# Kernel optimization log

Hardware: AMD Instinct MI355X
Metric: run time of the kernel (lower is better)

## Reference

```python
import jax, jax.numpy as jnp
import numpy as np

B, S_SRC, D, H, DH, FF, L, V, W, NG = 2, 4093, 768, 12, 64, 3072, 2, 50265, 256, 3
S = S_SRC + NG            # 4096, multiple of one-sided window W=256
NC = S // W               # 16 chunks
EPS = 1e-5
CLS_IDS = (50261, 50262, 50263)
NEG = -1e9


def setup_inputs() -> dict:
    key = jax.random.key(0)
    ks = jax.random.split(key, 16)
    std = 0.02
    inp = {
        "src": jax.random.randint(ks[0], (B, S_SRC), 0, 50260),
        "mask_src": jnp.ones((B, S_SRC), dtype=bool),
        "cluster_sizes": jax.random.randint(ks[1], (B,), 0, 16),
        "word_emb": jax.random.normal(ks[2], (V, D), jnp.float32) * std,
        "pos_emb": jax.random.normal(ks[3], (S, D), jnp.float32) * std,
        "emb_ln": jnp.stack([jnp.ones((D,)), jnp.zeros((D,))]),              # [2,D] scale,bias
        "attn_w": jax.random.normal(ks[4], (L, 7, D, D), jnp.float32) * std,  # q,k,v,qg,kg,vg,o
        "attn_b": jnp.zeros((L, 7, D), jnp.float32),
        "ln_p": jnp.stack([jnp.stack([jnp.ones((D,)), jnp.zeros((D,)), jnp.ones((D,)), jnp.zeros((D,))]) for _ in range(L)]),  # [L,4,D]
        "ffn_w1": jax.random.normal(ks[5], (L, D, FF), jnp.float32) * std,
        "ffn_b1": jnp.zeros((L, FF), jnp.float32),
        "ffn_w2": jax.random.normal(ks[6], (L, FF, D), jnp.float32) * std,
        "ffn_b2": jnp.zeros((L, D), jnp.float32),
        "cls_w": jax.random.normal(ks[7], (3, D), jnp.float32) * std,
        "cls_b": jnp.zeros((3,), jnp.float32),
    }
    return inp


def _ln(x, scale, bias):
    mu = jnp.mean(x, axis=-1, keepdims=True)
    var = jnp.mean(jnp.square(x - mu), axis=-1, keepdims=True)
    return (x - mu) * jax.lax.rsqrt(var + EPS) * scale + bias


def _encoder(ids, mask, word_emb, pos_emb, emb_ln, attn_w, attn_b, ln_p,
             ffn_w1, ffn_b1, ffn_w2, ffn_b2):
    x = _ln(word_emb[ids] + pos_emb[None, :S], emb_ln[0], emb_ln[1])  # [B,S,D]

    # static banded-attention index structure (chunk of W queries sees 3W keys)
    idx = np.arange(NC)[:, None] * W + np.arange(3 * W)[None, :]  # into padded seq
    kp = idx - W                                                   # absolute key pos
    valid = (kp >= 0) & (kp < S)
    kpc = jnp.asarray(np.clip(kp, 0, S - 1))
    qpos = np.arange(W)[:, None]
    band = jnp.asarray(np.abs(np.arange(3 * W)[None, :] - W - qpos) <= W)  # [W,3W]
    # global & padding keys removed from windowed attention (HF semantics)
    keymask = mask[:, kpc] & jnp.asarray(valid)[None] & jnp.asarray(kp >= NG)[None]  # [B,NC,3W]
    allowed = band[None, None] & keymask[:, :, None, :]  # [B,NC,W,3W]
    scale = 1.0 / np.sqrt(DH)

    def layer(x, p):
        aw, ab, lnp, w1, b1, w2, b2 = p
        def proj(i):
            return (x @ aw[i] + ab[i]).reshape(B, S, H, DH).transpose(0, 2, 1, 3)
        q = proj(0) * scale
        k = proj(1)
        v = proj(2)
        kpad = jnp.pad(k, ((0, 0), (0, 0), (W, W), (0, 0)))
        vpad = jnp.pad(v, ((0, 0), (0, 0), (W, W), (0, 0)))
        Kc = kpad[:, :, kpc + W]  # [B,H,NC,3W,DH] (kpc+W indexes padded)
        Vc = vpad[:, :, kpc + W]
        qc = q.reshape(B, H, NC, W, DH)
        s_loc = jnp.einsum('bhcqd,bhckd->bhcqk', qc, Kc)
        s_loc = jnp.where(allowed[:, None], s_loc, NEG)
        s_glb = jnp.einsum('bhcqd,bhgd->bhcqg', qc, k[:, :, :NG])  # all tokens -> global keys
        probs = jax.nn.softmax(jnp.concatenate([s_glb, s_loc], axis=-1), axis=-1)
        out = (jnp.einsum('bhcqg,bhgd->bhcqd', probs[..., :NG], v[:, :, :NG])
               + jnp.einsum('bhcqk,bhckd->bhcqd', probs[..., NG:], Vc))
        out = out.reshape(B, H, S, DH)
        # global query rows: full attention with global q/k/v projections
        qg = ((x[:, :NG] @ aw[3] + ab[3]).reshape(B, NG, H, DH)) * scale
        kg = (x @ aw[4] + ab[4]).reshape(B, S, H, DH)
        vg = (x @ aw[5] + ab[5]).reshape(B, S, H, DH)
        sg = jnp.einsum('bghd,bshd->bhgs', qg, kg)
        sg = jnp.where(mask[:, None, None, :], sg, NEG)
        og = jnp.einsum('bhgs,bshd->bhgd', jax.nn.softmax(sg, axis=-1), vg)
        out = out.at[:, :, :NG, :].set(og)
        out = out.transpose(0, 2, 1, 3).reshape(B, S, D)
        xa = _ln(x + out @ aw[6] + ab[6], lnp[0], lnp[1])
        h = jax.nn.gelu(xa @ w1 + b1, approximate=False)
        return _ln(xa + h @ w2 + b2, lnp[2], lnp[3]), None

    x, _ = jax.lax.scan(layer, x, (attn_w, attn_b, ln_p, ffn_w1, ffn_b1, ffn_w2, ffn_b2))
    return x


def reference(src, mask_src, cluster_sizes, word_emb, pos_emb, emb_ln, attn_w,
              attn_b, ln_p, ffn_w1, ffn_b1, ffn_w2, ffn_b2, cls_w, cls_b):
    ids = jnp.concatenate([jnp.broadcast_to(jnp.asarray(CLS_IDS), (B, NG)), src], axis=1)
    mask = jnp.concatenate([jnp.ones((B, NG), dtype=bool), mask_src], axis=1)
    h = _encoder(ids, mask, word_emb, pos_emb, emb_ln, attn_w, attn_b, ln_p,
                 ffn_w1, ffn_b1, ffn_w2, ffn_b2)  # [B,S,D]
    mf = mask.astype(h.dtype)
    scores = [jax.nn.sigmoid(h[:, i] @ cls_w[i] + cls_b[i]) * mf[:, i] for i in range(3)]
    verd, pros, cons = (s[:, None] for s in scores)
    return verd, pros, cons, mf[:, 0][:, None]
```

## Files before the change

kernel.cpp:

```cpp
#include <hip/hip_runtime.h>
#include <hip/hip_bf16.h>
#include <math.h>

#define B_    2
#define SSRC_ 4093
#define D_    768
#define H_    12
#define DH_   64
#define FF_   3072
#define NG_   3
#define W_    256
#define S_    4096
#define NC_   16
#define NSPLIT_ 16
#define QB_   128

typedef __attribute__((ext_vector_type(8))) short frag_ab;
typedef __attribute__((ext_vector_type(4))) float f32x4;

#define GL16(gp, lp) __builtin_amdgcn_global_load_lds( \
    (const __attribute__((address_space(1))) void*)(gp), \
    (__attribute__((address_space(3))) void*)(lp), 16, 0, 0)

__device__ __forceinline__ float bflo(unsigned int w) {
    union { float f; unsigned int i; } c; c.i = w << 16; return c.f;
}
__device__ __forceinline__ float bfhi(unsigned int w) {
    union { float f; unsigned int i; } c; c.i = w & 0xffff0000u; return c.f;
}
__device__ __forceinline__ void unp8(uint4 t, float* o) {
    o[0] = bflo(t.x); o[1] = bfhi(t.x); o[2] = bflo(t.y); o[3] = bfhi(t.y);
    o[4] = bflo(t.z); o[5] = bfhi(t.z); o[6] = bflo(t.w); o[7] = bfhi(t.w);
}
__device__ __forceinline__ unsigned short f2bfu(float x) {
    __hip_bfloat16 h = __float2bfloat16(x);
    return *reinterpret_cast<unsigned short*>(&h);
}

__device__ __forceinline__ float block_sum(float v, float* red) {
    int tid = threadIdx.x;
    red[tid] = v;
    __syncthreads();
#pragma unroll
    for (int off = 128; off >= 1; off >>= 1) {
        if (tid < off) red[tid] += red[tid + off];
        __syncthreads();
    }
    float r = red[0];
    __syncthreads();
    return r;
}

__device__ __forceinline__ float block_max(float v, float* red) {
    int tid = threadIdx.x;
    red[tid] = v;
    __syncthreads();
#pragma unroll
    for (int off = 128; off >= 1; off >>= 1) {
        if (tid < off) red[tid] = fmaxf(red[tid], red[tid + off]);
        __syncthreads();
    }
    float r = red[0];
    __syncthreads();
    return r;
}

__device__ __forceinline__ void storeO(float* p, float v) { *p = v; }
__device__ __forceinline__ void storeO(__hip_bfloat16* p, float v) { *p = __float2bfloat16(v); }

__global__ __launch_bounds__(256) void embed_ln_k(
    const int* __restrict__ src, const float* __restrict__ we,
    const float* __restrict__ pe, const float* __restrict__ gam,
    const float* __restrict__ bet, float* __restrict__ X,
    __hip_bfloat16* __restrict__ Xb) {
    __shared__ float red[256];
    int row = blockIdx.x;
    int b = row >> 12;
    int s = row & (S_ - 1);
    int tid = threadIdx.x;
    int id = (s < NG_) ? (50261 + s) : src[b * SSRC_ + (s - NG_)];
    const float* wr = we + (size_t)id * D_;
    const float* pr = pe + (size_t)s * D_;
    float v[3];
    float lsum = 0.f;
#pragma unroll
    for (int j = 0; j < 3; ++j) {
        int c = tid + j * 256;
        v[j] = wr[c] + pr[c];
        lsum += v[j];
    }
    float mu = block_sum(lsum, red) * (1.0f / 768.0f);
    float ls2 = 0.f;
#pragma unroll
    for (int j = 0; j < 3; ++j) { float d = v[j] - mu; ls2 += d * d; }
    float var = block_sum(ls2, red) * (1.0f / 768.0f);
    float rs = rsqrtf(var + 1e-5f);
    float* xr = X + (size_t)row * D_;
    __hip_bfloat16* xbr = Xb + (size_t)row * D_;
#pragma unroll
    for (int j = 0; j < 3; ++j) {
        int c = tid + j * 256;
        float o = (v[j] - mu) * rs * gam[c] + bet[c];
        xr[c] = o;
        xbr[c] = __float2bfloat16(o);
    }
}

__global__ __launch_bounds__(256) void residual_ln_k(
    const float* __restrict__ x, const float* __restrict__ y,
    const float* __restrict__ y2, const float* __restrict__ gam,
    const float* __restrict__ bet, float* __restrict__ out,
    __hip_bfloat16* __restrict__ outb) {
    __shared__ float red[256];
    int row = blockIdx.x;
    int tid = threadIdx.x;
    const float* xr = x + (size_t)row * D_;
    const float* yr = y + (size_t)row * D_;
    const float* y2r = y2 ? y2 + (size_t)row * D_ : nullptr;
    float v[3];
    float lsum = 0.f;
#pragma unroll
    for (int j = 0; j < 3; ++j) {
        int c = tid + j * 256;
        v[j] = xr[c] + yr[c];
        if (y2r) v[j] += y2r[c];
        lsum += v[j];
    }
    float mu = block_sum(lsum, red) * (1.0f / 768.0f);
    float ls2 = 0.f;
#pragma unroll
    for (int j = 0; j < 3; ++j) { float d = v[j] - mu; ls2 += d * d; }
    float var = block_sum(ls2, red) * (1.0f / 768.0f);
    float rs = rsqrtf(var + 1e-5f);
    float* orow = out + (size_t)row * D_;
    __hip_bfloat16* obr = outb ? outb + (size_t)row * D_ : nullptr;
#pragma unroll
    for (int j = 0; j < 3; ++j) {
        int c = tid + j * 256;
        float o = (v[j] - mu) * rs * gam[c] + bet[c];
        orow[c] = o;
        if (obr) obr[c] = __float2bfloat16(o);
    }
}

__global__ __launch_bounds__(256) void convt_k(
    const float* __restrict__ W, __hip_bfloat16* __restrict__ WT,
    int K, int N, int npb ) {
    __shared__ float tile[32][33];
    int mat = blockIdx.x / npb;
    int bx = blockIdx.x - mat * npb;
    int by = blockIdx.y;
    const float* Wm = W + (size_t)mat * K * N;
    __hip_bfloat16* WTm = WT + (size_t)mat * N * K;
    int tx = threadIdx.x & 31, ty = threadIdx.x >> 5;
#pragma unroll
    for (int i = 0; i < 32; i += 8)
        tile[ty + i][tx] = Wm[(size_t)(by * 32 + ty + i) * N + bx * 32 + tx];
    __syncthreads();
#pragma unroll
    for (int i = 0; i < 32; i += 8)
        WTm[(size_t)(bx * 32 + ty + i) * K + by * 32 + tx] = __float2bfloat16(tile[tx][ty + i]);
}

__global__ void pack_bias_k(const float* __restrict__ ab, float* __restrict__ dst) {
    int j = blockIdx.x * 256 + threadIdx.x;
    if (j >= 5 * 768) return;
    int mat = j / 768, c = j - mat * 768;
    int i = (mat < 3) ? mat : mat + 1;
    dst[j] = ab[i * 768 + c];
}

template <int EPI, int SPLIT>
__global__ __launch_bounds__(256) void mfma_gemm_k(
    const __hip_bfloat16* __restrict__ A, const __hip_bfloat16* __restrict__ BT,
    const float* __restrict__ bias, void* __restrict__ Cout,
    int M, int N, int K, size_t matstride) {
    __shared__ __align__(16) __hip_bfloat16 As[2][4096];
    __shared__ __align__(16) __hip_bfloat16 Bs[2][4096];
    int tid = threadIdx.x;
    int lane = tid & 63;
    int w = tid >> 6, wr = w >> 1, wc = w & 1;
    int nwg = gridDim.x * gridDim.y;
    int id = blockIdx.y * gridDim.x + blockIdx.x;
    if ((nwg & 7) == 0) {
        int per = nwg >> 3;
        id = (id & 7) * per + (id >> 3);
    }
    int bx = id % gridDim.x, by = id / gridDim.x;
    int brow = by * 128, bcol = bx * 128;
    int z = blockIdx.z, nz = gridDim.z;
    int Kz = K / nz;
    int r0 = tid >> 2, k0 = (tid & 3) * 8;
    const __hip_bfloat16* Ag0 = A + (size_t)(brow + r0) * K + z * Kz + k0;
    const __hip_bfloat16* Ag1 = Ag0 + (size_t)64 * K;
    const __hip_bfloat16* Bg0 = BT + (size_t)(bcol + r0) * K + z * Kz + k0;
    const __hip_bfloat16* Bg1 = Bg0 + (size_t)64 * K;

    f32x4 acc[4][4];
#pragma unroll
    for (int m = 0; m < 4; ++m)
#pragma unroll
        for (int n = 0; n < 4; ++n) acc[m][n] = (f32x4){0.f, 0.f, 0.f, 0.f};

    int l15 = lane & 15, kb = lane >> 4;
    int aoff = (wr * 64 + l15) * 32 + kb * 8;
    int boff = (wc * 64 + l15) * 32 + kb * 8;

    int nt = Kz >> 5;
    GL16(Ag0, &As[0][tid * 8]);
    GL16(Ag1, &As[0][tid * 8 + 2048]);
    GL16(Bg0, &Bs[0][tid * 8]);
    GL16(Bg1, &Bs[0][tid * 8 + 2048]);
    __syncthreads();

    for (int t = 0; t < nt; ++t) {
        int cur = t & 1;
        if (t + 1 < nt) {
            int nxt = cur ^ 1;
            int kt = (t + 1) << 5;
            GL16(Ag0 + kt, &As[nxt][tid * 8]);
            GL16(Ag1 + kt, &As[nxt][tid * 8 + 2048]);
            GL16(Bg0 + kt, &Bs[nxt][tid * 8]);
            GL16(Bg1 + kt, &Bs[nxt][tid * 8 + 2048]);
        }
        frag_ab af[4], bf[4];
#pragma unroll
        for (int m = 0; m < 4; ++m) af[m] = *(const frag_ab*)&As[cur][aoff + m * 512];
#pragma unroll
        for (int n = 0; n < 4; ++n) bf[n] = *(const frag_ab*)&Bs[cur][boff + n * 512];
        __builtin_amdgcn_s_setprio(1);
#pragma unroll
        for (int m = 0; m < 4; ++m)
#pragma unroll
            for (int n = 0; n < 4; ++n)
                acc[m][n] = __builtin_amdgcn_mfma_f32_16x16x32_bf16(af[m], bf[n], acc[m][n], 0, 0, 0);
        __builtin_amdgcn_s_setprio(0);
        __syncthreads();
    }

    size_t zoff = (size_t)z * M * N;
#pragma unroll
    for (int m = 0; m < 4; ++m) {
        int rowb = brow + wr * 64 + m * 16 + (lane >> 4) * 4;
#pragma unroll
        for (int n = 0; n < 4; ++n) {
            int col = bcol + wc * 64 + n * 16 + l15;
            float bv = (z == 0) ? bias[col] : 0.f;
#pragma unroll
            for (int r = 0; r < 4; ++r) {
                float v = acc[m][n][r] + bv;
                size_t idx;
                if (SPLIT) {
                    int mat = col / 768;
                    idx = (size_t)mat * matstride + (size_t)(rowb + r) * 768 + (col - mat * 768);
                } else {
                    idx = zoff + (size_t)(rowb + r) * N + col;
                }
                if (EPI == 0) {
                    ((float*)Cout)[idx] = v;
                } else if (EPI == 1) {
                    ((__hip_bfloat16*)Cout)[idx] = __float2bfloat16(v);
                } else {
                    float g = 0.5f * v * (1.0f + erff(v * 0.70710678118654752f));
                    ((__hip_bfloat16*)Cout)[idx] = __float2bfloat16(g);
                }
            }
        }
    }
}

__global__ __launch_bounds__(256) void skinny_gemm_k(
    const float* __restrict__ A, const float* __restrict__ W,
    float* __restrict__ partial, int N, int K) {
    __shared__ float Asl[6][64];
    __shared__ float red[4][6][64];
    int tid = threadIdx.x;
    int cl = tid & 63;
    int kg = tid >> 6;
    int col = blockIdx.x * 64 + cl;
    int k0 = blockIdx.y * 64;
    for (int i = tid; i < 6 * 64; i += 256)
        Asl[i >> 6][i & 63] = A[(size_t)(i >> 6) * K + k0 + (i & 63)];
    __syncthreads();
    float acc[6] = {0.f, 0.f, 0.f, 0.f, 0.f, 0.f};
#pragma unroll
    for (int kk = 0; kk < 16; ++kk) {
        int k = kg * 16 + kk;
        float wv = W[(size_t)(k0 + k) * N + col];
#pragma unroll
        for (int m = 0; m < 6; ++m) acc[m] += Asl[m][k] * wv;
    }
#pragma unroll
    for (int m = 0; m < 6; ++m) red[kg][m][cl] = acc[m];
    __syncthreads();
    for (int i = tid; i < 6 * 64; i += 256) {
        int m = i >> 6, lane = i & 63;
        float s = red[0][m][lane] + red[1][m][lane] + red[2][m][lane] + red[3][m][lane];
        partial[(size_t)blockIdx.y * 6 * N + (size_t)m * N + blockIdx.x * 64 + lane] = s;
    }
}

__global__ __launch_bounds__(256) void skinny_reduce_k(
    const float* __restrict__ partial, const float* __restrict__ bias,
    float* __restrict__ outp, int N, int KS, int gelu) {
    int idx = blockIdx.x * 256 + threadIdx.x;
    if (idx >= 6 * N) return;
    int m = idx / N, col = idx - m * N;
    float s = bias[col];
    for (int kb = 0; kb < KS; ++kb)
        s += partial[(size_t)kb * 6 * N + (size_t)m * N + col];
    if (gelu) s = 0.5f * s * (1.0f + erff(s * 0.70710678118654752f));
    outp[(size_t)m * N + col] = s;
}

__global__ __launch_bounds__(256, 1) void local_attn_k(
    const __hip_bfloat16* __restrict__ Q, const __hip_bfloat16* __restrict__ K,
    const __hip_bfloat16* __restrict__ V, __hip_bfloat16* __restrict__ O) {
    __shared__ __align__(16) __hip_bfloat16 K_lds[64 * 72];
    __shared__ __align__(16) __hip_bfloat16 VT_lds[64 * 72];
    __shared__ __align__(16) __hip_bfloat16 P_lds[4][16 * 72];

    const int cq = blockIdx.x, h = blockIdx.y, b = blockIdx.z;
    const int tid = threadIdx.x;
    const int lane = tid & 63;
    const int w = tid >> 6;
    const int l15 = lane & 15, g4 = lane >> 4;
    const int cbase = cq * QB_;

    frag_ab qf[2][2];
#pragma unroll
    for (int qt = 0; qt < 2; ++qt) {
        int qa = cbase + w * 32 + qt * 16 + l15;
        const __hip_bfloat16* qp = Q + (size_t)(b * S_ + qa) * D_ + h * DH_ + g4 * 8;
        qf[qt][0] = *(const frag_ab*)qp;
        qf[qt][1] = *(const frag_ab*)(qp + 32);
    }

    f32x4 o[2][4];
#pragma unroll
    for (int qt = 0; qt < 2; ++qt)
#pragma unroll
        for (int dt = 0; dt < 4; ++dt) o[qt][dt] = (f32x4){0.f, 0.f, 0.f, 0.f};
    float mrun[2] = {-1e30f, -1e30f};
    float lrun[2] = {0.f, 0.f};

    int kw0 = cbase - W_; if (kw0 < 0) kw0 = 0;
    int kw1 = cbase + QB_ + W_; if (kw1 > S_) kw1 = S_;
    int ntiles = (kw1 - kw0) >> 6;

    char* Pw = (char*)P_lds[w];

    for (int t = 0; t < ntiles; ++t) {
        int k0 = kw0 + t * 64;
        __syncthreads();
        {
            const __hip_bfloat16* Kg = K + (size_t)(b * S_ + k0) * D_ + h * DH_;
            const __hip_bfloat16* Vg = V + (size_t)(b * S_ + k0) * D_ + h * DH_;
#pragma unroll
            for (int it = 0; it < 2; ++it) {
                int idx = tid + it * 256;
                int kk = idx >> 3, d0 = (idx & 7) * 8;
                uint4 kv = *(const uint4*)(Kg + (size_t)kk * D_ + d0);
                *(uint4*)&K_lds[kk * 72 + d0] = kv;
                uint4 vv = *(const uint4*)(Vg + (size_t)kk * D_ + d0);
                unsigned short vs[8];
                *(uint4*)vs = vv;
#pragma unroll
                for (int j = 0; j < 8; ++j) {
                    int dd = d0 + j;
                    int boff = dd * 144 + ((kk * 2) ^ (((dd >> 3) & 7) << 4));
                    *(unsigned short*)((char*)VT_lds + boff) = vs[j];
                }
            }
        }
        __syncthreads();

        frag_ab kf[4][2];
#pragma unroll
        for (int kt = 0; kt < 4; ++kt) {
            const char* kp = (const char*)K_lds + (kt * 16 + l15) * 144 + g4 * 16;
            kf[kt][0] = *(const frag_ab*)kp;
            kf[kt][1] = *(const frag_ab*)(kp + 64);
        }
        frag_ab vf[4][2];
#pragma unroll
        for (int dt = 0; dt < 4; ++dt) {
            int drow = dt * 16 + l15;
            int swz = ((drow >> 3) & 7) << 4;
            const char* vp = (const char*)VT_lds + drow * 144;
            vf[dt][0] = *(const frag_ab*)(vp + ((g4 * 16) ^ swz));
            vf[dt][1] = *(const frag_ab*)(vp + ((g4 * 16 + 64) ^ swz));
        }

#pragma unroll
        for (int qt = 0; qt < 2; ++qt) {
            f32x4 st[4];
            __builtin_amdgcn_s_setprio(1);
#pragma unroll
            for (int kt = 0; kt < 4; ++kt) {
                f32x4 z = (f32x4){0.f, 0.f, 0.f, 0.f};
                z = __builtin_amdgcn_mfma_f32_16x16x32_bf16(kf[kt][0], qf[qt][0], z, 0, 0, 0);
                z = __builtin_amdgcn_mfma_f32_16x16x32_bf16(kf[kt][1], qf[qt][1], z, 0, 0, 0);
                st[kt] = z;
            }
            __builtin_amdgcn_s_setprio(0);
            int qa = cbase + w * 32 + qt * 16 + l15;
            float sv[16];
            float mx = -1e30f;
#pragma unroll
            for (int kt = 0; kt < 4; ++kt)
#pragma unroll
                for (int r = 0; r < 4; ++r) {
                    int ka = k0 + kt * 16 + g4 * 4 + r;
                    float s = st[kt][r] * 0.125f;
                    bool bad = (ka < NG_) | (ka - qa > W_) | (qa - ka > W_);
                    s = bad ? -1e30f : s;
                    sv[kt * 4 + r] = s;
                    mx = fmaxf(mx, s);
                }
            mx = fmaxf(mx, __shfl_xor(mx, 16));
            mx = fmaxf(mx, __shfl_xor(mx, 32));
            float mnew = fmaxf(fmaxf(mrun[qt], mx), -60.0f);
            if (__any(mnew != mrun[qt])) {
                float fsc = __expf(mrun[qt] - mnew);
                mrun[qt] = mnew;
#pragma unroll
                for (int dt = 0; dt < 4; ++dt) o[qt][dt] *= fsc;
                lrun[qt] *= fsc;
            }
            float psum = 0.f;
            unsigned short pb[16];
#pragma unroll
            for (int i = 0; i < 16; ++i) {
                float p = __expf(sv[i] - mrun[qt]);
                psum += p;
                pb[i] = f2bfu(p);
            }
            psum += __shfl_xor(psum, 16);
            psum += __shfl_xor(psum, 32);
            lrun[qt] += psum;
#pragma unroll
            for (int kt = 0; kt < 4; ++kt)
#pragma unroll
                for (int rp = 0; rp < 2; ++rp) {
                    unsigned vpk = (unsigned)pb[kt * 4 + rp * 2] | ((unsigned)pb[kt * 4 + rp * 2 + 1] << 16);
                    int kloc = kt * 16 + g4 * 4 + rp * 2;
                    *(unsigned*)(Pw + l15 * 144 + kloc * 2) = vpk;
                }
            frag_ab pf0 = *(const frag_ab*)(Pw + l15 * 144 + g4 * 16);
            frag_ab pf1 = *(const frag_ab*)(Pw + l15 * 144 + g4 * 16 + 64);
            __builtin_amdgcn_s_setprio(1);
#pragma unroll
            for (int dt = 0; dt < 4; ++dt) {
                o[qt][dt] = __builtin_amdgcn_mfma_f32_16x16x32_bf16(vf[dt][0], pf0, o[qt][dt], 0, 0, 0);
                o[qt][dt] = __builtin_amdgcn_mfma_f32_16x16x32_bf16(vf[dt][1], pf1, o[qt][dt], 0, 0, 0);
            }
            __builtin_amdgcn_s_setprio(0);
        }
    }

    uint4 kgc[3][2];
    uint2 vgd[3][4];
#pragma unroll
    for (int gk = 0; gk < NG_; ++gk) {
        const __hip_bfloat16* kp = K + (size_t)(b * S_ + gk) * D_ + h * DH_ + g4 * 8;
        kgc[gk][0] = *(const uint4*)kp;
        kgc[gk][1] = *(const uint4*)(kp + 32);
        const __hip_bfloat16* vp = V + (size_t)(b * S_ + gk) * D_ + h * DH_ + g4 * 4;
#pragma unroll
        for (int dt = 0; dt < 4; ++dt)
            vgd[gk][dt] = *(const uint2*)(vp + dt * 16);
    }
#pragma unroll
    for (int qt = 0; qt < 2; ++qt) {
        float sg[3];
#pragma unroll
        for (int gk = 0; gk < NG_; ++gk) {
            float part = 0.f;
#pragma unroll
            for (int s = 0; s < 2; ++s) {
                uint4 qw = *(uint4*)&qf[qt][s];
                uint4 kw = kgc[gk][s];
                part += bflo(qw.x) * bflo(kw.x) + bfhi(qw.x) * bfhi(kw.x);
                part += bflo(qw.y) * bflo(kw.y) + bfhi(qw.y) * bfhi(kw.y);
                part += bflo(qw.z) * bflo(kw.z) + bfhi(qw.z) * bfhi(kw.z);
                part += bflo(qw.w) * bflo(kw.w) + bfhi(qw.w) * bfhi(kw.w);
            }
            part += __shfl_xor(part, 16);
            part += __shfl_xor(part, 32);
            sg[gk] = part * 0.125f;
        }
        float mx3 = fmaxf(fmaxf(sg[0], sg[1]), sg[2]);
        float mnew = fmaxf(fmaxf(mrun[qt], mx3), -60.0f);
        float fsc = __expf(mrun[qt] - mnew);
        mrun[qt] = mnew;
#pragma unroll
        for (int dt = 0; dt < 4; ++dt) o[qt][dt] *= fsc;
        lrun[qt] *= fsc;
        float pg[3];
        float psum = 0.f;
#pragma unroll
        for (int gk = 0; gk < NG_; ++gk) { pg[gk] = __expf(sg[gk] - mnew); psum += pg[gk]; }
        lrun[qt] += psum;
#pragma unroll
        for (int dt = 0; dt < 4; ++dt) {
#pragma unroll
            for (int gk = 0; gk < NG_; ++gk) {
                uint2 vv = vgd[gk][dt];
                o[qt][dt][0] += pg[gk] * bflo(vv.x);
                o[qt][dt][1] += pg[gk] * bfhi(vv.x);
                o[qt][dt][2] += pg[gk] * bflo(vv.y);
                o[qt][dt][3] += pg[gk] * bfhi(vv.y);
            }
        }
    }

#pragma unroll
    for (int qt = 0; qt < 2; ++qt) {
        float linv = 1.0f / lrun[qt];
        int qa = cbase + w * 32 + qt * 16 + l15;
        __hip_bfloat16* orow = O + (size_t)(b * S_ + qa) * D_ + h * DH_;
#pragma unroll
        for (int dt = 0; dt < 4; ++dt) {
            unsigned short pk[4];
#pragma unroll
            for (int r = 0; r < 4; ++r) pk[r] = f2bfu(o[qt][dt][r] * linv);
            *(uint2*)(orow + dt * 16 + g4 * 4) = *(uint2*)pk;
        }
    }
}

__global__ __launch_bounds__(256) void gattn_part_k(
    const float* __restrict__ qg, const __hip_bfloat16* __restrict__ KG,
    const __hip_bfloat16* __restrict__ VG, float* __restrict__ gpart) {
    __shared__ float sc[256];
    __shared__ float qs[DH_];
    __shared__ float red[256];
    __shared__ float rv[16][64];
    int split = blockIdx.x;
    int gh = blockIdx.y;
    int g = gh / H_, h = gh - g * H_;
    int b = blockIdx.z;
    int tid = threadIdx.x;
    if (tid < DH_) qs[tid] = qg[(size_t)(b * NG_ + g) * D_ + h * DH_ + tid] * 0.125f;
    __syncthreads();
    int s0 = split * (S_ / NSPLIT_);
    float acc = 0.f;
    {
        const __hip_bfloat16* kp = KG + (size_t)(b * S_ + s0 + tid) * D_ + h * DH_;
#pragma unroll
        for (int c8 = 0; c8 < 8; ++c8) {
            uint4 t = *(const uint4*)(kp + c8 * 8);
            float f[8]; unp8(t, f);
#pragma unroll
            for (int j = 0; j < 8; ++j) acc += qs[c8 * 8 + j] * f[j];
        }
    }
    float m = block_max(acc, red);
    float e = __expf(acc - m);
    sc[tid] = e;
    float l = block_sum(e, red);
    int sgq = tid >> 4, dq = (tid & 15) * 4;
    float a0 = 0.f, a1 = 0.f, a2 = 0.f, a3 = 0.f;
    const __hip_bfloat16* vbase = VG + (size_t)(b * S_ + s0 + sgq * 16) * D_ + h * DH_ + dq;
#pragma unroll
    for (int i = 0; i < 16; ++i) {
        float p = sc[sgq * 16 + i];
        uint2 vv = *(const uint2*)(vbase + (size_t)i * D_);
        a0 += p * bflo(vv.x); a1 += p * bfhi(vv.x);
        a2 += p * bflo(vv.y); a3 += p * bfhi(vv.y);
    }
    rv[sgq][dq] = a0; rv[sgq][dq + 1] = a1; rv[sgq][dq + 2] = a2; rv[sgq][dq + 3] = a3;
    __syncthreads();
    float* op = gpart + ((size_t)((b * NG_ + g) * H_ + h) * NSPLIT_ + split) * 66;
    if (tid == 0) { op[0] = m; op[1] = l; }
    if (tid < DH_) {
        float s = 0.f;
#pragma unroll
        for (int j = 0; j < 16; ++j) s += rv[j][tid];
        op[2 + tid] = s;
    }
}

template <typename TO>
__global__ __launch_bounds__(64) void gattn_comb_k(
    const float* __restrict__ gpart, TO* __restrict__ outp, int rowStride) {
    int g = blockIdx.x, h = blockIdx.y, b = blockIdx.z;
    int tid = threadIdx.x;
    const float* base = gpart + (size_t)((b * NG_ + g) * H_ + h) * NSPLIT_ * 66;
    float M = -1e30f;
#pragma unroll
    for (int p = 0; p < NSPLIT_; ++p) M = fmaxf(M, base[p * 66]);
    float l = 0.f, o = 0.f;
#pragma unroll
    for (int p = 0; p < NSPLIT_; ++p) {
        float wgt = __expf(base[p * 66] - M);
        l += wgt * base[p * 66 + 1];
        o += wgt * base[p * 66 + 2 + tid];
    }
    storeO(&outp[(size_t)(b * rowStride + g) * D_ + h * DH_ + tid], o / l);
}

__global__ void gather6_k(const float* __restrict__ X, float* __restrict__ xg) {
    int r = blockIdx.x;
    int b = r / NG_, g = r % NG_;
    for (int c = threadIdx.x; c < D_; c += blockDim.x)
        xg[(size_t)r * D_ + c] = X[(size_t)(b * S_ + g) * D_ + c];
}

__global__ __launch_bounds__(256) void classifier_k(
    const float* __restrict__ x26, const float* __restrict__ cw,
    const float* __restrict__ cb, float* __restrict__ out) {
    __shared__ float red[256];
    int tid = threadIdx.x;
    for (int i = 0; i < 3; ++i) {
        for (int b = 0; b < B_; ++b) {
            const float* xr = x26 + (size_t)(b * NG_ + i) * D_;
            const float* wr = cw + (size_t)i * D_;
            float p = 0.f;
            for (int c = tid; c < D_; c += 256) p += xr[c] * wr[c];
            float dotv = block_sum(p, red);
            if (tid == 0) out[i * B_ + b] = 1.0f / (1.0f + __expf(-(dotv + cb[i])));
        }
    }
    if (tid == 0) { out[6] = 1.0f; out[7] = 1.0f; }
}

extern "C" void kernel_launch(void* const* d_in, const int* in_sizes, int n_in,
                              void* d_out, int out_size, void* d_ws, size_t ws_size,
                              hipStream_t stream) {
    const int*   src      = (const int*)d_in[0];
    const float* word_emb = (const float*)d_in[3];
    const float* pos_emb  = (const float*)d_in[4];
    const float* emb_ln   = (const float*)d_in[5];
    const float* attn_w   = (const float*)d_in[6];
    const float* attn_b   = (const float*)d_in[7];
    const float* ln_p     = (const float*)d_in[8];
    const float* ffn_w1   = (const float*)d_in[9];
    const float* ffn_b1   = (const float*)d_in[10];
    const float* ffn_w2   = (const float*)d_in[11];
    const float* ffn_b2   = (const float*)d_in[12];
    const float* cls_w    = (const float*)d_in[13];
    const float* cls_b    = (const float*)d_in[14];
    float* out = (float*)d_out;

    const size_t NT = (size_t)B_ * S_ * D_;
    float* base = (float*)d_ws;
    float* X  = base;
    float* P4 = base + NT;
    __hip_bfloat16* Xb  = (__hip_bfloat16*)(base + 2 * NT);
    __hip_bfloat16* Qb  = (__hip_bfloat16*)(base + 5 * NT / 2);
    __hip_bfloat16* Kb  = (__hip_bfloat16*)(base + 3 * NT);
    __hip_bfloat16* Vb  = (__hip_bfloat16*)(base + 7 * NT / 2);
    __hip_bfloat16* KGb = (__hip_bfloat16*)(base + 4 * NT);
    __hip_bfloat16* VGb = (__hip_bfloat16*)(base + 9 * NT / 2);
    __hip_bfloat16* AOb = (__hip_bfloat16*)(base + 5 * NT);
    __hip_bfloat16* HCb = (__hip_bfloat16*)(base + 11 * NT / 2);
    float* pj1 = base + 15 * NT / 2;
    float* pj2 = base + 17 * NT / 2;
    __hip_bfloat16* wq5 = (__hip_bfloat16*)(base + 19 * NT / 2);
    __hip_bfloat16* wo  = wq5 + 5 * 589824;
    __hip_bfloat16* wg1 = wo + 589824;
    __hip_bfloat16* wf1 = wg1 + 2 * 589824;
    __hip_bfloat16* wf2 = wf1 + 2359296;
    float* SM  = (float*)(wf2 + 2359296);
    float* xg  = SM;
    float* qg6 = xg + 6 * D_;
    float* og6 = qg6 + 6 * D_;
    float* pr6 = og6 + 6 * D_;
    float* xa6 = pr6 + 6 * D_;
    float* h6  = xa6 + 6 * D_;
    float* f6  = h6 + 6 * FF_;
    float* x26 = f6 + 6 * D_;
    float* bias5 = x26 + 6 * D_;
    float* part = bias5 + 5 * D_;
    float* gpart = part;

    const int M = B_ * S_;
    dim3 blk(256);

    auto aw = [&](int l, int i) { return attn_w + ((size_t)(l * 7 + i)) * D_ * D_; };
    auto ab = [&](int l, int i) { return attn_b + (size_t)(l * 7 + i) * D_; };
    auto lnp = [&](int l, int i) { return ln_p + (size_t)(l * 4 + i) * D_; };

    auto skinny = [&](const float* A6, const float* Wm, const float* bias,
                      float* out6, int N, int K, int gelu) {
        skinny_gemm_k<<<dim3(N / 64, K / 64), blk, 0, stream>>>(A6, Wm, part, N, K);
        skinny_reduce_k<<<dim3((6 * N + 255) / 256), blk, 0, stream>>>(part, bias, out6, N, K / 64, gelu);
    };

    embed_ln_k<<<M, blk, 0, stream>>>(src, word_emb, pos_emb, emb_ln, emb_ln + D_, X, Xb);

    convt_k<<<dim3(24 * 3, 24), blk, 0, stream>>>(aw(0, 0), wq5, D_, D_, 24);
    convt_k<<<dim3(24 * 2, 24), blk, 0, stream>>>(aw(0, 4), wq5 + 3 * 589824, D_, D_, 24);
    pack_bias_k<<<15, blk, 0, stream>>>(ab(0, 0), bias5);
    mfma_gemm_k<1, 1><<<dim3(3840 / 128, 64), blk, 0, stream>>>(Xb, wq5, bias5, Qb, M, 3840, D_, NT);
    local_attn_k<<<dim3(S_ / QB_, H_, B_), blk, 0, stream>>>(Qb, Kb, Vb, AOb);
    gather6_k<<<B_ * NG_, blk, 0, stream>>>(X, xg);
    skinny(xg, aw(0, 3), ab(0, 3), qg6, D_, D_, 0);
    gattn_part_k<<<dim3(NSPLIT_, NG_ * H_, B_), blk, 0, stream>>>(qg6, KGb, VGb, gpart);
    gattn_comb_k<__hip_bfloat16><<<dim3(NG_, H_, B_), dim3(64), 0, stream>>>(gpart, AOb, S_);
    convt_k<<<dim3(24, 24), blk, 0, stream>>>(aw(0, 6), wo, D_, D_, 24);
    mfma_gemm_k<0, 0><<<dim3(6, 64, 2), blk, 0, stream>>>(AOb, wo, ab(0, 6), pj1, M, D_, D_, 0);
    residual_ln_k<<<M, blk, 0, stream>>>(X, pj1, pj2, lnp(0, 0), lnp(0, 1), P4, Xb);
    convt_k<<<dim3(96, 24), blk, 0, stream>>>(ffn_w1, wf1, D_, FF_, 96);
    convt_k<<<dim3(24, 96), blk, 0, stream>>>(ffn_w2, wf2, FF_, D_, 24);
    mfma_gemm_k<2, 0><<<dim3(24, 64), blk, 0, stream>>>(Xb, wf1, ffn_b1, HCb, M, FF_, D_, 0);
    mfma_gemm_k<0, 0><<<dim3(6, 64, 2), blk, 0, stream>>>(HCb, wf2, ffn_b2, pj1, M, D_, FF_, 0);
    residual_ln_k<<<M, blk, 0, stream>>>(P4, pj1, pj2, lnp(0, 2), lnp(0, 3), X, Xb);

    convt_k<<<dim3(24 * 2, 24), blk, 0, stream>>>(aw(1, 4), wg1, D_, D_, 24);
    mfma_gemm_k<1, 1><<<dim3(1536 / 128, 64), blk, 0, stream>>>(Xb, wg1, ab(1, 4), KGb, M, 1536, D_, NT);
    gather6_k<<<B_ * NG_, blk, 0, stream>>>(X, xg);
    skinny(xg, aw(1, 3), ab(1, 3), qg6, D_, D_, 0);
    gattn_part_k<<<dim3(NSPLIT_, NG_ * H_, B_), blk, 0, stream>>>(qg6, KGb, VGb, gpart);
    gattn_comb_k<float><<<dim3(NG_, H_, B_), dim3(64), 0, stream>>>(gpart, og6, NG_);
    skinny(og6, aw(1, 6), ab(1, 6), pr6, D_, D_, 0);
    residual_ln_k<<<B_ * NG_, blk, 0, stream>>>(xg, pr6, nullptr, lnp(1, 0), lnp(1, 1), xa6, nullptr);
    skinny(xa6, ffn_w1 + (size_t)D_ * FF_, ffn_b1 + FF_, h6, FF_, D_, 1);
    skinny(h6, ffn_w2 + (size_t)FF_ * D_, ffn_b2 + D_, f6, D_, FF_, 0);
    residual_ln_k<<<B_ * NG_, blk, 0, stream>>>(xa6, f6, nullptr, lnp(1, 2), lnp(1, 3), x26, nullptr);
    classifier_k<<<1, blk, 0, stream>>>(x26, cls_w, cls_b, out);
}
```

Before: 504.9 us.

## Add 256x256-tile MFMA GEMM for QKV and FFN1 projections

Introduces a 512-thread GEMM kernel with 256x256 output tiles, double-buffered LDS loads via global_load_lds, and an XCD-aware block remap. It replaces the 128-tile GEMM for the fused QKV/global projection and the FFN up-projection with GELU. Larger tiles raise arithmetic intensity and cut redundant global loads, but use more registers and LDS per block and launch fewer workgroups (15x32 and 12x32), which may reduce occupancy and leave CUs less evenly loaded.

New measurement: 537.4 us. +6.4%, slower.

```diff
diff --git a/kernel.cpp b/kernel.cpp
--- a/kernel.cpp
+++ b/kernel.cpp
@@ -255,6 +255,103 @@
                     idx = (size_t)mat * matstride + (size_t)(rowb + r) * 768 + (col - mat * 768);
                 } else {
                     idx = zoff + (size_t)(rowb + r) * N + col;
+                }
+                if (EPI == 0) {
+                    ((float*)Cout)[idx] = v;
+                } else if (EPI == 1) {
+                    ((__hip_bfloat16*)Cout)[idx] = __float2bfloat16(v);
+                } else {
+                    float g = 0.5f * v * (1.0f + erff(v * 0.70710678118654752f));
+                    ((__hip_bfloat16*)Cout)[idx] = __float2bfloat16(g);
+                }
+            }
+        }
+    }
+}
+
+template <int EPI, int SPLIT>
+__global__ __launch_bounds__(512) void mfma_gemm256_k(
+    const __hip_bfloat16* __restrict__ A, const __hip_bfloat16* __restrict__ BT,
+    const float* __restrict__ bias, void* __restrict__ Cout,
+    int M, int N, int K, size_t matstride) {
+    __shared__ __align__(16) __hip_bfloat16 As[2][8192];
+    __shared__ __align__(16) __hip_bfloat16 Bs[2][8192];
+    int tid = threadIdx.x;
+    int lane = tid & 63;
+    int w = tid >> 6;
+    int wr = w >> 2, wc = w & 3;
+    int nwg = gridDim.x * gridDim.y;
+    int id = blockIdx.y * gridDim.x + blockIdx.x;
+    if ((nwg & 7) == 0) {
+        int per = nwg >> 3;
+        id = (id & 7) * per + (id >> 3);
+    }
+    int bx = id % gridDim.x, by = id / gridDim.x;
+    int brow = by * 256, bcol = bx * 256;
+    int r0 = tid >> 2, k0 = (tid & 3) * 8;
+    const __hip_bfloat16* Ag0 = A + (size_t)(brow + r0) * K + k0;
+    const __hip_bfloat16* Ag1 = Ag0 + (size_t)128 * K;
+    const __hip_bfloat16* Bg0 = BT + (size_t)(bcol + r0) * K + k0;
+    const __hip_bfloat16* Bg1 = Bg0 + (size_t)128 * K;
+
+    f32x4 acc[8][4];
+#pragma unroll
+    for (int m = 0; m < 8; ++m)
+#pragma unroll
+        for (int n = 0; n < 4; ++n) acc[m][n] = (f32x4){0.f, 0.f, 0.f, 0.f};
+
+    int l15 = lane & 15, kb = lane >> 4;
+    int aoff = (wr * 128 + l15) * 32 + kb * 8;
+    int boff = (wc * 64 + l15) * 32 + kb * 8;
+
+    int nt = K >> 5;
+    GL16(Ag0, &As[0][tid * 8]);
+    GL16(Ag1, &As[0][tid * 8 + 4096]);
+    GL16(Bg0, &Bs[0][tid * 8]);
+    GL16(Bg1, &Bs[0][tid * 8 + 4096]);
+    __syncthreads();
+
+    for (int t = 0; t < nt; ++t) {
+        int cur = t & 1;
+        if (t + 1 < nt) {
+            int nxt = cur ^ 1;
+            int kt = (t + 1) << 5;
+            GL16(Ag0 + kt, &As[nxt][tid * 8]);
+            GL16(Ag1 + kt, &As[nxt][tid * 8 + 4096]);
+            GL16(Bg0 + kt, &Bs[nxt][tid * 8]);
+            GL16(Bg1 + kt, &Bs[nxt][tid * 8 + 4096]);
+        }
+        frag_ab bf[4];
+#pragma unroll
+        for (int n = 0; n < 4; ++n) bf[n] = *(const frag_ab*)&Bs[cur][boff + n * 512];
+        __builtin_amdgcn_s_setprio(1);
+#pragma unroll
+        for (int m = 0; m < 8; ++m) {
+            frag_ab af = *(const frag_ab*)&As[cur][aoff + m * 512];
+#pragma unroll
+            for (int n = 0; n < 4; ++n)
+                acc[m][n] = __builtin_amdgcn_mfma_f32_16x16x32_bf16(af, bf[n], acc[m][n], 0, 0, 0);
+        }
+        __builtin_amdgcn_s_setprio(0);
+        __syncthreads();
+    }
+
+#pragma unroll
+    for (int m = 0; m < 8; ++m) {
+        int rowb = brow + wr * 128 + m * 16 + (lane >> 4) * 4;
+#pragma unroll
+        for (int n = 0; n < 4; ++n) {
+            int col = bcol + wc * 64 + n * 16 + l15;
+            float bv = bias[col];
+#pragma unroll
+            for (int r = 0; r < 4; ++r) {
+                float v = acc[m][n][r] + bv;
+                size_t idx;
+                if (SPLIT) {
+                    int mat = col / 768;
+                    idx = (size_t)mat * matstride + (size_t)(rowb + r) * 768 + (col - mat * 768);
+                } else {
+                    idx = (size_t)(rowb + r) * N + col;
                 }
                 if (EPI == 0) {
                     ((float*)Cout)[idx] = v;
@@ -694,7 +791,7 @@
     convt_k<<<dim3(24 * 3, 24), blk, 0, stream>>>(aw(0, 0), wq5, D_, D_, 24);
     convt_k<<<dim3(24 * 2, 24), blk, 0, stream>>>(aw(0, 4), wq5 + 3 * 589824, D_, D_, 24);
     pack_bias_k<<<15, blk, 0, stream>>>(ab(0, 0), bias5);
-    mfma_gemm_k<1, 1><<<dim3(3840 / 128, 64), blk, 0, stream>>>(Xb, wq5, bias5, Qb, M, 3840, D_, NT);
+    mfma_gemm256_k<1, 1><<<dim3(3840 / 256, M / 256), dim3(512), 0, stream>>>(Xb, wq5, bias5, Qb, M, 3840, D_, NT);
     local_attn_k<<<dim3(S_ / QB_, H_, B_), blk, 0, stream>>>(Qb, Kb, Vb, AOb);
     gather6_k<<<B_ * NG_, blk, 0, stream>>>(X, xg);
     skinny(xg, aw(0, 3), ab(0, 3), qg6, D_, D_, 0);
@@ -705,7 +802,7 @@
     residual_ln_k<<<M, blk, 0, stream>>>(X, pj1, pj2, lnp(0, 0), lnp(0, 1), P4, Xb);
     convt_k<<<dim3(96, 24), blk, 0, stream>>>(ffn_w1, wf1, D_, FF_, 96);
     convt_k<<<dim3(24, 96), blk, 0, stream>>>(ffn_w2, wf2, FF_, D_, 24);
-    mfma_gemm_k<2, 0><<<dim3(24, 64), blk, 0, stream>>>(Xb, wf1, ffn_b1, HCb, M, FF_, D_, 0);
+    mfma_gemm256_k<2, 0><<<dim3(FF_ / 256, M / 256), dim3(512), 0, stream>>>(Xb, wf1, ffn_b1, HCb, M, FF_, D_, 0);
     mfma_gemm_k<0, 0><<<dim3(6, 64, 2), blk, 0, stream>>>(HCb, wf2, ffn_b2, pj1, M, D_, FF_, 0);
     residual_ln_k<<<M, blk, 0, stream>>>(P4, pj1, pj2, lnp(0, 2), lnp(0, 3), X, Xb);
 
```
